# Optimization experiments

Hardware: AMD Instinct MI355X
Metric: run time of the kernel (lower is better)

## Reference

```python
import jax, jax.numpy as jnp
import numpy as np

ALPHA = 0.2          # LeakyReLU negative slope
NEG_INF = -9e15      # mask value from the original code


def setup_inputs() -> dict:
    key = jax.random.key(0)
    k1, k2, k3, k4 = jax.random.split(key, 4)
    B, N, F_in, F_out = 8, 2048, 64, 64
    x = jax.random.normal(k1, (B, N, F_in), dtype=jnp.float32)
    adj = jax.random.randint(k2, (B, N, N), 0, 2, dtype=jnp.int32)
    W = jax.random.normal(k3, (F_in, F_out), dtype=jnp.float32)
    a = jax.random.normal(k4, (2 * F_out, 1), dtype=jnp.float32)
    return {"x": x, "adj": adj, "W": W, "a": a}


def reference(x, adj, W, a):
    # h: [B, N, F_out]
    h = jnp.matmul(x, W)
    F_out = W.shape[1]
    a1 = a[:F_out, 0]   # source half of attention vector
    a2 = a[F_out:, 0]   # target half
    # e_ij = leakyrelu(h_i . a1 + h_j . a2)  -- identical math to the
    # original cat([h_i, h_j]) @ a without materializing [B,N*N,2F].
    s1 = jnp.einsum('bnf,f->bn', h, a1)  # [B, N]
    s2 = jnp.einsum('bnf,f->bn', h, a2)  # [B, N]
    e = jax.nn.leaky_relu(s1[:, :, None] + s2[:, None, :], negative_slope=ALPHA)
    masked = jnp.where(adj > 0, e, NEG_INF)
    attention = jax.nn.softmax(masked, axis=2)  # [B, N, N]
    # dropout p=0.0 / eval mode -> identity
    h_prime = jnp.matmul(attention, h)          # [B, N, F_out]
    return jax.nn.elu(h_prime)                  # concat=True branch
```

## Files before the change

### kernel.cpp

```cpp
#include <hip/hip_runtime.h>
#include <cstdint>

#define LRELU_ALPHA 0.2f
#define NEG_INF -9000000000000000.0f
#define L2E 1.4426950408889634f

typedef __bf16 bf16x8 __attribute__((ext_vector_type(8)));
typedef unsigned short ushortx8 __attribute__((ext_vector_type(8)));
typedef float floatx4 __attribute__((ext_vector_type(4)));

constexpr int Bb = 8, Nn = 2048, Ff = 64;
constexpr int TJ = 64;
constexpr int LSTR = 72;
constexpr int SEG = 8;
constexpr int SEGT = (Nn / TJ) / SEG;
constexpr int NROWS = Bb * Nn;

__device__ __forceinline__ unsigned short f2bf(float f) {
    unsigned u = __builtin_bit_cast(unsigned, f);
    u = u + 0x7FFFu + ((u >> 16) & 1u);
    return (unsigned short)(u >> 16);
}

__global__ __launch_bounds__(256) void gat_prep(
    const float* __restrict__ x, const float* __restrict__ W, const float* __restrict__ a,
    unsigned short* __restrict__ hT, float* __restrict__ s1g, float* __restrict__ s2g)
{
    constexpr int STR2 = 36;
    __shared__ unsigned short hblk[64 * STR2];
    const int tid = threadIdx.x;
    const int blk = blockIdx.x;
    const int b  = blk >> 6;
    const int i0 = (blk & 63) * 32;
    const int w    = tid >> 6;
    const int lane = tid & 63;

    float wcol[64];
    #pragma unroll
    for (int k = 0; k < 64; ++k) wcol[k] = W[k * 64 + lane];
    const float a1 = a[lane], a2 = a[64 + lane];

    for (int r = 0; r < 8; ++r) {
        const int il = w * 8 + r;
        const int i  = i0 + il;
        const float* xrow = x + ((size_t)(b * Nn + i)) * 64;
        float h = 0.f;
        #pragma unroll
        for (int k = 0; k < 64; ++k) h = fmaf(xrow[k], wcol[k], h);
        float p1 = h * a1, p2 = h * a2;
        #pragma unroll
        for (int off = 32; off; off >>= 1) {
            p1 += __shfl_xor(p1, off);
            p2 += __shfl_xor(p2, off);
        }
        if (lane == 0) { s1g[b * Nn + i] = p1; s2g[b * Nn + i] = p2; }
        hblk[lane * STR2 + il] = f2bf(h);
    }
    __syncthreads();
    {
        const int f = tid >> 2, c = (tid & 3) * 8;
        uint4 v = *reinterpret_cast<const uint4*>(&hblk[f * STR2 + c]);
        *reinterpret_cast<uint4*>(hT + ((size_t)b * 64 + f) * Nn + i0 + c) = v;
    }
}

__global__ __launch_bounds__(128) void gat_attn(
    const int* __restrict__ adj, const unsigned short* __restrict__ hT,
    const float* __restrict__ s1g, const float* __restrict__ s2g,
    float* __restrict__ m_part, float* __restrict__ l_part, float* __restrict__ O_part)
{
    __shared__ unsigned short hT_lds[64 * LSTR];
    __shared__ float s2_lds[TJ];

    const int tid  = threadIdx.x;
    const int blk  = blockIdx.x;
    const int seg  = blk >> 9;
    const int grp  = blk & 511;
    const int gr0  = grp * 32;
    const int b    = gr0 >> 11;
    const int i0   = gr0 & 2047;
    const int w    = tid >> 6;
    const int lane = tid & 63;
    const int fl   = lane & 15;
    const int q    = lane >> 4;

    const int i = i0 + w * 16 + fl;
    const float s1v = s1g[b * Nn + i];
    const int* adj_row = adj + ((size_t)(b * Nn + i)) * Nn;
    const unsigned short* hTb = hT + (size_t)b * 64 * Nn;
    const float* s2b = s2g + b * Nn;

    float m = NEG_INF, l = 0.f;
    floatx4 C[4] = {};

    const int sf = tid >> 1, sc = (tid & 1) * 32;

    const int jt0 = seg * SEGT;

    int4 adjv[4];
    {
        const int* arow = adj_row + jt0 * TJ;
        const int4* ap0 = reinterpret_cast<const int4*>(arow + q * 8);
        adjv[0] = ap0[0]; adjv[1] = ap0[1];
        const int4* ap1 = reinterpret_cast<const int4*>(arow + 32 + q * 8);
        adjv[2] = ap1[0]; adjv[3] = ap1[1];
    }

    for (int jt = jt0; jt < jt0 + SEGT; ++jt) {
        const int j0 = jt * TJ;
        __syncthreads();
        {
            const uint4* gsrc = reinterpret_cast<const uint4*>(hTb + (size_t)sf * Nn + j0 + sc);
            uint4 g0 = gsrc[0], g1 = gsrc[1], g2 = gsrc[2], g3 = gsrc[3];
            uint4* ldst = reinterpret_cast<uint4*>(&hT_lds[sf * LSTR + sc]);
            ldst[0] = g0; ldst[1] = g1; ldst[2] = g2; ldst[3] = g3;
            if (tid < TJ) s2_lds[tid] = s2b[j0 + tid];
        }
        __syncthreads();

        int4 nadj[4] = {};
        if (jt + 1 < jt0 + SEGT) {
            const int* nrow = adj_row + j0 + TJ;
            const int4* ap0 = reinterpret_cast<const int4*>(nrow + q * 8);
            nadj[0] = ap0[0]; nadj[1] = ap0[1];
            const int4* ap1 = reinterpret_cast<const int4*>(nrow + 32 + q * 8);
            nadj[2] = ap1[0]; nadj[3] = ap1[1];
        }

        float e[16];
        const int* av = reinterpret_cast<const int*>(adjv);
        #pragma unroll
        for (int t = 0; t < 2; ++t) {
            float s2v[8];
            *reinterpret_cast<float4*>(&s2v[0]) =
                *reinterpret_cast<const float4*>(&s2_lds[t * 32 + q * 8]);
            *reinterpret_cast<float4*>(&s2v[4]) =
                *reinterpret_cast<const float4*>(&s2_lds[t * 32 + q * 8 + 4]);
            #pragma unroll
            for (int jj = 0; jj < 8; ++jj) {
                float ev = s1v + s2v[jj];
                ev = fmaxf(ev, LRELU_ALPHA * ev);
                e[t * 8 + jj] = (av[t * 8 + jj] > 0) ? ev : NEG_INF;
            }
        }
        float tmax = e[0];
        #pragma unroll
        for (int k = 1; k < 16; ++k) tmax = fmaxf(tmax, e[k]);
        tmax = fmaxf(tmax, __shfl_xor(tmax, 16));
        tmax = fmaxf(tmax, __shfl_xor(tmax, 32));
        const float m_new = fmaxf(m, tmax);
        const float alpha_s = exp2f((m - m_new) * L2E);
        m = m_new;

        float tsum = 0.f;
        float p[16];
        #pragma unroll
        for (int k = 0; k < 16; ++k) {
            p[k] = exp2f((e[k] - m_new) * L2E);
            tsum += p[k];
        }
        tsum += __shfl_xor(tsum, 16);
        tsum += __shfl_xor(tsum, 32);
        l = l * alpha_s + tsum;

        ushortx8 a0v, a1v;
#if __has_builtin(__builtin_amdgcn_cvt_pk_bf16_f32)
        #pragma unroll
        for (int jj = 0; jj < 4; ++jj) {
            ushortx8* dst = jj < 2 ? &a0v : &a1v;
        }
        #pragma unroll
        for (int jj = 0; jj < 8; ++jj) { a0v[jj] = f2bf(p[jj]); a1v[jj] = f2bf(p[8 + jj]); }
#else
        #pragma unroll
        for (int jj = 0; jj < 8; ++jj) { a0v[jj] = f2bf(p[jj]); a1v[jj] = f2bf(p[8 + jj]); }
#endif
        const bf16x8 A0 = __builtin_bit_cast(bf16x8, a0v);
        const bf16x8 A1 = __builtin_bit_cast(bf16x8, a1v);

        float ac[4];
        #pragma unroll
        for (int r = 0; r < 4; ++r) ac[r] = __shfl(alpha_s, q * 4 + r);
        #pragma unroll
        for (int u = 0; u < 4; ++u)
            #pragma unroll
            for (int r = 0; r < 4; ++r) C[u][r] *= ac[r];

        #pragma unroll
        for (int u = 0; u < 4; ++u) {
            const bf16x8 B0 = *reinterpret_cast<const bf16x8*>(
                &hT_lds[(u * 16 + fl) * LSTR + q * 8]);
            C[u] = __builtin_amdgcn_mfma_f32_16x16x32_bf16(A0, B0, C[u], 0, 0, 0);
            const bf16x8 B1 = *reinterpret_cast<const bf16x8*>(
                &hT_lds[(u * 16 + fl) * LSTR + 32 + q * 8]);
            C[u] = __builtin_amdgcn_mfma_f32_16x16x32_bf16(A1, B1, C[u], 0, 0, 0);
        }
        adjv[0] = nadj[0]; adjv[1] = nadj[1]; adjv[2] = nadj[2]; adjv[3] = nadj[3];
    }

    if (q == 0) {
        const int ri = b * Nn + i;
        m_part[seg * NROWS + ri] = m;
        l_part[seg * NROWS + ri] = l;
    }
    #pragma unroll
    for (int u = 0; u < 4; ++u) {
        #pragma unroll
        for (int r = 0; r < 4; ++r) {
            const int orow = i0 + w * 16 + q * 4 + r;
            O_part[((size_t)seg * NROWS + b * Nn + orow) * 64 + u * 16 + fl] = C[u][r];
        }
    }
}

__global__ __launch_bounds__(256) void gat_merge(
    const float* __restrict__ m_part, const float* __restrict__ l_part,
    const float* __restrict__ O_part, float* __restrict__ out)
{
    const int tid = threadIdx.x;
    const int ri  = blockIdx.x * 4 + (tid >> 6);
    const int f   = tid & 63;

    float mv[SEG];
    #pragma unroll
    for (int s = 0; s < SEG; ++s) mv[s] = m_part[s * NROWS + ri];
    float mstar = mv[0];
    #pragma unroll
    for (int s = 1; s < SEG; ++s) mstar = fmaxf(mstar, mv[s]);

    float lsum = 0.f, acc = 0.f;
    #pragma unroll
    for (int s = 0; s < SEG; ++s) {
        const float wgt = exp2f((mv[s] - mstar) * L2E);
        lsum += l_part[s * NROWS + ri] * wgt;
        acc  += O_part[((size_t)s * NROWS + ri) * 64 + f] * wgt;
    }
    float v = acc / lsum;
    v = (v > 0.f) ? v : (exp2f(v * L2E) - 1.f);
    out[(size_t)ri * 64 + f] = v;
}

extern "C" void kernel_launch(void* const* d_in, const int* in_sizes, int n_in,
                              void* d_out, int out_size, void* d_ws, size_t ws_size,
                              hipStream_t stream) {
    const float* x   = (const float*)d_in[0];
    const int*   adj = (const int*)d_in[1];
    const float* W   = (const float*)d_in[2];
    const float* a   = (const float*)d_in[3];
    float* out = (float*)d_out;

    char* p = (char*)d_ws;
    unsigned short* hT = (unsigned short*)p;  p += (size_t)Bb * 64 * Nn * sizeof(unsigned short);
    float* s1 = (float*)p;                    p += (size_t)NROWS * sizeof(float);
    float* s2 = (float*)p;                    p += (size_t)NROWS * sizeof(float);
    float* m_part = (float*)p;                p += (size_t)SEG * NROWS * sizeof(float);
    float* l_part = (float*)p;                p += (size_t)SEG * NROWS * sizeof(float);
    float* O_part = (float*)p;

    gat_prep<<<dim3(Bb * Nn / 32), dim3(256), 0, stream>>>(x, W, a, hT, s1, s2);
    gat_attn<<<dim3(SEG * (Bb * Nn / 32)), dim3(128), 0, stream>>>(
        adj, hT, s1, s2, m_part, l_part, O_part);
    gat_merge<<<dim3(NROWS / 4), dim3(256), 0, stream>>>(m_part, l_part, O_part, out);
}
```

Before: 237.7 us.

## Stage full segment window of hT in LDS once with 256-thread blocks

The attention kernel now loads the whole per-segment window of the transposed bf16 h matrix (256 columns) and s2 into LDS once, instead of reloading a 64-column tile with two barriers per iteration. Blocks grow to 256 threads covering 64 rows, so each staged tile is shared by four waves. The change also uses the packed v_cvt_pk_bf16_f32 instruction for probability conversion, raises wave priority around the MFMA block, and splits the prep kernel's dot product into four accumulators. The cost is more LDS per block (about 34 KB) and a larger up-front load before compute starts, which may lower occupancy.

```diff
diff --git a/kernel.cpp b/kernel.cpp
--- a/kernel.cpp
+++ b/kernel.cpp
@@ -8,18 +8,26 @@
 typedef __bf16 bf16x8 __attribute__((ext_vector_type(8)));
 typedef unsigned short ushortx8 __attribute__((ext_vector_type(8)));
 typedef float floatx4 __attribute__((ext_vector_type(4)));
+typedef unsigned int uintx4 __attribute__((ext_vector_type(4)));
 
 constexpr int Bb = 8, Nn = 2048, Ff = 64;
 constexpr int TJ = 64;
-constexpr int LSTR = 72;
 constexpr int SEG = 8;
 constexpr int SEGT = (Nn / TJ) / SEG;
+constexpr int WIN = SEGT * TJ;
+constexpr int WSTR = 264;
 constexpr int NROWS = Bb * Nn;
 
 __device__ __forceinline__ unsigned short f2bf(float f) {
     unsigned u = __builtin_bit_cast(unsigned, f);
     u = u + 0x7FFFu + ((u >> 16) & 1u);
     return (unsigned short)(u >> 16);
+}
+
+__device__ __forceinline__ unsigned cvt_pk_bf16(float lo, float hi) {
+    unsigned r;
+    asm("v_cvt_pk_bf16_f32 %0, %1, %2" : "=v"(r) : "v"(lo), "v"(hi));
+    return r;
 }
 
 __global__ __launch_bounds__(256) void gat_prep(
@@ -44,9 +52,15 @@
         const int il = w * 8 + r;
         const int i  = i0 + il;
         const float* xrow = x + ((size_t)(b * Nn + i)) * 64;
-        float h = 0.f;
-        #pragma unroll
-        for (int k = 0; k < 64; ++k) h = fmaf(xrow[k], wcol[k], h);
+        float h0 = 0.f, h1 = 0.f, h2 = 0.f, h3 = 0.f;
+        #pragma unroll
+        for (int k = 0; k < 64; k += 4) {
+            h0 = fmaf(xrow[k],     wcol[k],     h0);
+            h1 = fmaf(xrow[k + 1], wcol[k + 1], h1);
+            h2 = fmaf(xrow[k + 2], wcol[k + 2], h2);
+            h3 = fmaf(xrow[k + 3], wcol[k + 3], h3);
+        }
+        const float h = (h0 + h1) + (h2 + h3);
         float p1 = h * a1, p2 = h * a2;
         #pragma unroll
         for (int off = 32; off; off >>= 1) {
@@ -64,19 +78,19 @@
     }
 }
 
-__global__ __launch_bounds__(128) void gat_attn(
+__global__ __launch_bounds__(256) void gat_attn(
     const int* __restrict__ adj, const unsigned short* __restrict__ hT,
     const float* __restrict__ s1g, const float* __restrict__ s2g,
     float* __restrict__ m_part, float* __restrict__ l_part, float* __restrict__ O_part)
 {
-    __shared__ unsigned short hT_lds[64 * LSTR];
-    __shared__ float s2_lds[TJ];
+    __shared__ unsigned short hT_lds[64 * WSTR];
+    __shared__ float s2_lds[WIN];
 
     const int tid  = threadIdx.x;
     const int blk  = blockIdx.x;
-    const int seg  = blk >> 9;
-    const int grp  = blk & 511;
-    const int gr0  = grp * 32;
+    const int seg  = blk >> 8;
+    const int grp  = blk & 255;
+    const int gr0  = grp * 64;
     const int b    = gr0 >> 11;
     const int i0   = gr0 & 2047;
     const int w    = tid >> 6;
@@ -85,67 +99,71 @@
     const int q    = lane >> 4;
 
     const int i = i0 + w * 16 + fl;
+    const int j0w = seg * WIN;
+    const unsigned short* hTb = hT + (size_t)b * 64 * Nn;
+
+    uint4 stg[8];
+    #pragma unroll
+    for (int k = 0; k < 8; ++k) {
+        const int c = tid + (k << 8);
+        stg[k] = *reinterpret_cast<const uint4*>(
+            hTb + (size_t)(c >> 5) * Nn + j0w + ((c & 31) << 3));
+    }
+    const float s2stg = s2g[b * Nn + j0w + tid];
     const float s1v = s1g[b * Nn + i];
     const int* adj_row = adj + ((size_t)(b * Nn + i)) * Nn;
-    const unsigned short* hTb = hT + (size_t)b * 64 * Nn;
-    const float* s2b = s2g + b * Nn;
-
-    float m = NEG_INF, l = 0.f;
-    floatx4 C[4] = {};
-
-    const int sf = tid >> 1, sc = (tid & 1) * 32;
-
-    const int jt0 = seg * SEGT;
 
     int4 adjv[4];
     {
-        const int* arow = adj_row + jt0 * TJ;
+        const int* arow = adj_row + j0w;
         const int4* ap0 = reinterpret_cast<const int4*>(arow + q * 8);
         adjv[0] = ap0[0]; adjv[1] = ap0[1];
         const int4* ap1 = reinterpret_cast<const int4*>(arow + 32 + q * 8);
         adjv[2] = ap1[0]; adjv[3] = ap1[1];
     }
 
-    for (int jt = jt0; jt < jt0 + SEGT; ++jt) {
-        const int j0 = jt * TJ;
-        __syncthreads();
-        {
-            const uint4* gsrc = reinterpret_cast<const uint4*>(hTb + (size_t)sf * Nn + j0 + sc);
-            uint4 g0 = gsrc[0], g1 = gsrc[1], g2 = gsrc[2], g3 = gsrc[3];
-            uint4* ldst = reinterpret_cast<uint4*>(&hT_lds[sf * LSTR + sc]);
-            ldst[0] = g0; ldst[1] = g1; ldst[2] = g2; ldst[3] = g3;
-            if (tid < TJ) s2_lds[tid] = s2b[j0 + tid];
-        }
-        __syncthreads();
+    #pragma unroll
+    for (int k = 0; k < 8; ++k) {
+        const int c = tid + (k << 8);
+        *reinterpret_cast<uint4*>(&hT_lds[(c >> 5) * WSTR + ((c & 31) << 3)]) = stg[k];
+    }
+    s2_lds[tid] = s2stg;
+    __syncthreads();
+
+    float m = NEG_INF, l = 0.f;
+    floatx4 C[4] = {};
+
+    for (int jt = 0; jt < SEGT; ++jt) {
+        const int jloc = jt * TJ;
 
         int4 nadj[4] = {};
-        if (jt + 1 < jt0 + SEGT) {
-            const int* nrow = adj_row + j0 + TJ;
+        if (jt + 1 < SEGT) {
+            const int* nrow = adj_row + j0w + jloc + TJ;
             const int4* ap0 = reinterpret_cast<const int4*>(nrow + q * 8);
             nadj[0] = ap0[0]; nadj[1] = ap0[1];
             const int4* ap1 = reinterpret_cast<const int4*>(nrow + 32 + q * 8);
             nadj[2] = ap1[0]; nadj[3] = ap1[1];
         }
 
-        float e[16];
+        float p[16];
         const int* av = reinterpret_cast<const int*>(adjv);
         #pragma unroll
         for (int t = 0; t < 2; ++t) {
             float s2v[8];
             *reinterpret_cast<float4*>(&s2v[0]) =
-                *reinterpret_cast<const float4*>(&s2_lds[t * 32 + q * 8]);
+                *reinterpret_cast<const float4*>(&s2_lds[jloc + t * 32 + q * 8]);
             *reinterpret_cast<float4*>(&s2v[4]) =
-                *reinterpret_cast<const float4*>(&s2_lds[t * 32 + q * 8 + 4]);
+                *reinterpret_cast<const float4*>(&s2_lds[jloc + t * 32 + q * 8 + 4]);
             #pragma unroll
             for (int jj = 0; jj < 8; ++jj) {
                 float ev = s1v + s2v[jj];
                 ev = fmaxf(ev, LRELU_ALPHA * ev);
-                e[t * 8 + jj] = (av[t * 8 + jj] > 0) ? ev : NEG_INF;
+                p[t * 8 + jj] = (av[t * 8 + jj] > 0) ? ev : NEG_INF;
             }
         }
-        float tmax = e[0];
-        #pragma unroll
-        for (int k = 1; k < 16; ++k) tmax = fmaxf(tmax, e[k]);
+        float tmax = p[0];
+        #pragma unroll
+        for (int k = 1; k < 16; ++k) tmax = fmaxf(tmax, p[k]);
         tmax = fmaxf(tmax, __shfl_xor(tmax, 16));
         tmax = fmaxf(tmax, __shfl_xor(tmax, 32));
         const float m_new = fmaxf(m, tmax);
@@ -153,30 +171,23 @@
         m = m_new;
 
         float tsum = 0.f;
-        float p[16];
         #pragma unroll
         for (int k = 0; k < 16; ++k) {
-            p[k] = exp2f((e[k] - m_new) * L2E);
+            p[k] = exp2f((p[k] - m_new) * L2E);
             tsum += p[k];
         }
         tsum += __shfl_xor(tsum, 16);
         tsum += __shfl_xor(tsum, 32);
         l = l * alpha_s + tsum;
 
-        ushortx8 a0v, a1v;
-#if __has_builtin(__builtin_amdgcn_cvt_pk_bf16_f32)
-        #pragma unroll
-        for (int jj = 0; jj < 4; ++jj) {
-            ushortx8* dst = jj < 2 ? &a0v : &a1v;
-        }
-        #pragma unroll
-        for (int jj = 0; jj < 8; ++jj) { a0v[jj] = f2bf(p[jj]); a1v[jj] = f2bf(p[8 + jj]); }
-#else
-        #pragma unroll
-        for (int jj = 0; jj < 8; ++jj) { a0v[jj] = f2bf(p[jj]); a1v[jj] = f2bf(p[8 + jj]); }
-#endif
-        const bf16x8 A0 = __builtin_bit_cast(bf16x8, a0v);
-        const bf16x8 A1 = __builtin_bit_cast(bf16x8, a1v);
+        uintx4 pa, pb;
+        #pragma unroll
+        for (int d = 0; d < 4; ++d) {
+            pa[d] = cvt_pk_bf16(p[2 * d],     p[2 * d + 1]);
+            pb[d] = cvt_pk_bf16(p[8 + 2 * d], p[8 + 2 * d + 1]);
+        }
+        const bf16x8 A0 = __builtin_bit_cast(bf16x8, pa);
+        const bf16x8 A1 = __builtin_bit_cast(bf16x8, pb);
 
         float ac[4];
         #pragma unroll
@@ -186,15 +197,18 @@
             #pragma unroll
             for (int r = 0; r < 4; ++r) C[u][r] *= ac[r];
 
+        __builtin_amdgcn_s_setprio(1);
         #pragma unroll
         for (int u = 0; u < 4; ++u) {
             const bf16x8 B0 = *reinterpret_cast<const bf16x8*>(
-                &hT_lds[(u * 16 + fl) * LSTR + q * 8]);
+                &hT_lds[(u * 16 + fl) * WSTR + jloc + q * 8]);
             C[u] = __builtin_amdgcn_mfma_f32_16x16x32_bf16(A0, B0, C[u], 0, 0, 0);
             const bf16x8 B1 = *reinterpret_cast<const bf16x8*>(
-                &hT_lds[(u * 16 + fl) * LSTR + 32 + q * 8]);
+                &hT_lds[(u * 16 + fl) * WSTR + jloc + 32 + q * 8]);
             C[u] = __builtin_amdgcn_mfma_f32_16x16x32_bf16(A1, B1, C[u], 0, 0, 0);
         }
+        __builtin_amdgcn_s_setprio(0);
+
         adjv[0] = nadj[0]; adjv[1] = nadj[1]; adjv[2] = nadj[2]; adjv[3] = nadj[3];
     }
 
@@ -258,7 +272,7 @@
     float* O_part = (float*)p;
 
     gat_prep<<<dim3(Bb * Nn / 32), dim3(256), 0, stream>>>(x, W, a, hT, s1, s2);
-    gat_attn<<<dim3(SEG * (Bb * Nn / 32)), dim3(128), 0, stream>>>(
+    gat_attn<<<dim3(SEG * (NROWS / 64)), dim3(256), 0, stream>>>(
         adj, hT, s1, s2, m_part, l_part, O_part);
     gat_merge<<<dim3(NROWS / 4), dim3(256), 0, stream>>>(m_part, l_part, O_part, out);
 }
```

Result: no change. 237.0 us (-0.3%).
